# Kernel tuning notes

Hardware: AMD Instinct MI355X
Metric: run time of the kernel (lower is better)

## Reference

```python
import jax, jax.numpy as jnp
import numpy as np

D_MODEL = 2048
N_HEADS = 16
HEAD_DIM = D_MODEL // N_HEADS
B, L = 2, 2048
ROPE_BASE = 10000.0
NEG_INF = -1e30


def _rope_cache(seq_len, head_dim):
    inv_freq = 1.0 / (ROPE_BASE ** (np.arange(0, head_dim, 2, dtype=np.float32) / head_dim))
    t = np.arange(seq_len, dtype=np.float32)
    freqs = np.outer(t, inv_freq)                      # (L, hd/2)
    emb = np.concatenate([freqs, freqs], axis=-1)      # (L, hd)
    return jnp.asarray(np.cos(emb)), jnp.asarray(np.sin(emb))


def setup_inputs() -> dict:
    key = jax.random.key(0)
    kx, kq, ko, kl = jax.random.split(key, 4)
    x = jax.random.normal(kx, (B, L, D_MODEL), dtype=jnp.float32)
    w_qkv = jax.random.normal(kq, (3 * D_MODEL, D_MODEL), dtype=jnp.float32) / np.sqrt(D_MODEL)
    w_out = jax.random.normal(ko, (D_MODEL, D_MODEL), dtype=jnp.float32) / np.sqrt(D_MODEL)
    # key-padding style keep-mask: keep first `lengths[b]` tokens (pos 0 always kept)
    lengths = jax.random.randint(kl, (B,), L // 2, L + 1)
    attn_keep_mask = jnp.arange(L)[None, :] < lengths[:, None]
    cos, sin = _rope_cache(L, HEAD_DIM)
    return {"x": x, "attn_keep_mask": attn_keep_mask, "cos": cos, "sin": sin,
            "w_qkv": w_qkv, "w_out": w_out}


def _rotate_half(t):
    h = t.shape[-1] // 2
    return jnp.concatenate([-t[..., h:], t[..., :h]], axis=-1)


def _apply_rope(t, cos, sin):
    # t: (B, H, L, hd); cos/sin: (L, hd)
    return t * cos[None, None] + _rotate_half(t) * sin[None, None]


def reference(x, attn_keep_mask, cos, sin, w_qkv, w_out):
    Bv, Lv, Dv = x.shape
    qkv = jnp.einsum('bld,ed->ble', x, w_qkv)                      # (B, L, 3D)
    q, k, v = jnp.split(qkv, 3, axis=-1)
    def heads(t):
        return t.reshape(Bv, Lv, N_HEADS, HEAD_DIM).transpose(0, 2, 1, 3)  # (B,H,L,hd)
    q, k, v = heads(q), heads(k), heads(v)
    q = _apply_rope(q, cos, sin)
    k = _apply_rope(k, cos, sin)
    scale = 1.0 / np.sqrt(HEAD_DIM)
    scores = jnp.einsum('bhqd,bhkd->bhqk', q, k) * scale            # (B,H,L,L)
    causal = jnp.tril(jnp.ones((Lv, Lv), dtype=bool))               # (L,L)
    allowed = causal[None, None] & attn_keep_mask[:, None, None, :]  # keep keys
    scores = jnp.where(allowed, scores, NEG_INF)
    probs = jax.nn.softmax(scores, axis=-1)
    attn = jnp.einsum('bhqk,bhkd->bhqd', probs, v)                  # (B,H,L,hd)
    out = attn.transpose(0, 2, 1, 3).reshape(Bv, Lv, Dv)
    out = jnp.where(attn_keep_mask[:, :, None], out, 0.0)
    return jnp.einsum('bld,ed->ble', out, w_out)
```

## Files before the change

kernel.cpp:

```cpp
#include <hip/hip_runtime.h>

typedef unsigned short u16;
typedef u16 u16x8 __attribute__((ext_vector_type(8)));
typedef u16 u16x4 __attribute__((ext_vector_type(4)));
typedef __bf16 bf16x8_t __attribute__((ext_vector_type(8)));
typedef float f32x4 __attribute__((ext_vector_type(4)));

#define GLOBAL_AS __attribute__((address_space(1)))
#define LDS_AS __attribute__((address_space(3)))

__device__ __forceinline__ float bf2f(u16 v) {
    return __uint_as_float(((unsigned int)v) << 16);
}
__device__ __forceinline__ u16 f2bf(float f) {
    unsigned int u = __float_as_uint(f);
    u += 0x7fff + ((u >> 16) & 1);
    return (u16)(u >> 16);
}

__device__ __forceinline__ f32x4 mfma_bf16(u16x8 a, u16x8 b, f32x4 c) {
    return __builtin_amdgcn_mfma_f32_16x16x32_bf16(
        __builtin_bit_cast(bf16x8_t, a), __builtin_bit_cast(bf16x8_t, b), c, 0, 0, 0);
}

__device__ __forceinline__ float red16_max(float x) {
    int t;
    t = __builtin_amdgcn_update_dpp(0, __builtin_bit_cast(int, x), 0xB1, 0xF, 0xF, true);
    x = fmaxf(x, __builtin_bit_cast(float, t));
    t = __builtin_amdgcn_update_dpp(0, __builtin_bit_cast(int, x), 0x4E, 0xF, 0xF, true);
    x = fmaxf(x, __builtin_bit_cast(float, t));
    t = __builtin_amdgcn_update_dpp(0, __builtin_bit_cast(int, x), 0x124, 0xF, 0xF, true);
    x = fmaxf(x, __builtin_bit_cast(float, t));
    t = __builtin_amdgcn_update_dpp(0, __builtin_bit_cast(int, x), 0x128, 0xF, 0xF, true);
    x = fmaxf(x, __builtin_bit_cast(float, t));
    return x;
}

__global__ __launch_bounds__(256) void cvt_kernel(const float* __restrict__ in,
                                                  u16* __restrict__ out, int n4) {
    int i = blockIdx.x * 256 + threadIdx.x;
    if (i >= n4) return;
    float4 f = ((const float4*)in)[i];
    u16x4 o = { f2bf(f.x), f2bf(f.y), f2bf(f.z), f2bf(f.w) };
    ((u16x4*)out)[i] = o;
}

__global__ __launch_bounds__(256) void mask_prep(const unsigned char* __restrict__ raw,
                                                 int* __restrict__ lens) {
    const int b = blockIdx.x;
    const int tid = threadIdx.x, lane = tid & 63, wid = tid >> 6;
    const unsigned char b0 = raw[0];
    int cnt = 0;
    for (int i = tid; i < 2048; i += 256) {
        const size_t idx = (size_t)b * 2048 + i;
        bool v;
        if (b0 == 0) {
            v = ((const float*)raw)[idx] != 0.0f;
        } else if (b0 == 0x80) {
            v = ((const u16*)raw)[idx] != 0;
        } else {
            const int stride = raw[1] ? 1 : (raw[2] ? 2 : (raw[4] ? 4 : 8));
            v = raw[idx * stride] != 0;
        }
        cnt += v ? 1 : 0;
    }
    cnt += __shfl_xor(cnt, 1);
    cnt += __shfl_xor(cnt, 2);
    cnt += __shfl_xor(cnt, 4);
    cnt += __shfl_xor(cnt, 8);
    cnt += __shfl_xor(cnt, 16);
    cnt += __shfl_xor(cnt, 32);
    __shared__ int wsum[4];
    if (lane == 0) wsum[wid] = cnt;
    __syncthreads();
    if (tid == 0) lens[b] = wsum[0] + wsum[1] + wsum[2] + wsum[3];
}

template <int MODE>
__global__ __launch_bounds__(512, 2) void gemm_bt(
    const u16* __restrict__ A, const u16* __restrict__ B,
    int M, int N, int K, int rbx,
    u16* __restrict__ qp, u16* __restrict__ kp, u16* __restrict__ vp,
    float* __restrict__ outf) {
    __shared__ u16 lds[2 * 24576];
    const int tid  = threadIdx.x;
    const int lane = tid & 63;
    const int wid  = tid >> 6;
    const int wr   = wid >> 2;
    const int wc   = wid & 3;

    const int bid = blockIdx.x;
    const int k8  = bid & 7;
    const int loc = bid >> 3;
    const int by  = (k8 >> 2) * 16 + (loc & 15);
    const int bx  = (k8 & 3) * rbx + (loc >> 4);
    const int brow = by * 128;
    const int bcol = bx * 256;

    f32x4 acc[4][4];
#pragma unroll
    for (int m = 0; m < 4; ++m)
#pragma unroll
        for (int n = 0; n < 4; ++n)
            acc[m][n] = (f32x4){0.f, 0.f, 0.f, 0.f};

    const int s5   = (lane & 7) ^ (lane >> 3);
    const int srow = (wid << 4) + 2 * (lane >> 3) + (s5 >> 2);
    const int scol = (s5 & 3) << 3;
    const u16* aS = A + (size_t)(brow + srow) * K + scol;
    const u16* bS = B + (size_t)(bcol + srow) * K + scol;

    auto stgA = [&](int kt, int kh, int bb) {
        __builtin_amdgcn_global_load_lds(
            (const GLOBAL_AS void*)(aS + (size_t)kt * 64 + kh * 32),
            (LDS_AS void*)((char*)lds + bb * 49152 + kh * 8192 + wid * 1024), 16, 0, 0);
    };
    auto stgB = [&](int kt, int kh, int bb) {
        const u16* src = bS + (size_t)kt * 64 + kh * 32;
        char* base = (char*)lds + bb * 49152 + 16384 + kh * 16384 + wid * 1024;
        __builtin_amdgcn_global_load_lds((const GLOBAL_AS void*)src,
            (LDS_AS void*)base, 16, 0, 0);
        __builtin_amdgcn_global_load_lds((const GLOBAL_AS void*)(src + (size_t)128 * K),
            (LDS_AS void*)(base + 8192), 16, 0, 0);
    };

    auto rdA = [&](int bb, int kh, int mi) -> u16x8 {
        const int r  = wr * 64 + mi * 16 + (lane & 15);
        const int pr = r >> 1;
        const int g  = (((r & 1) << 2) + (lane >> 4)) ^ (pr & 7);
        return *(const u16x8*)((const char*)lds + bb * 49152 + kh * 8192 + pr * 128 + g * 16);
    };
    auto rdB = [&](int bb, int kh, int ni) -> u16x8 {
        const int r  = wc * 64 + ni * 16 + (lane & 15);
        const int pr = r >> 1;
        const int g  = (((r & 1) << 2) + (lane >> 4)) ^ (pr & 7);
        return *(const u16x8*)((const char*)lds + bb * 49152 + 16384 + kh * 16384 + pr * 128 + g * 16);
    };

    const int nkt = K >> 6;
    stgA(0, 0, 0); stgB(0, 0, 0);
    stgA(0, 1, 0); stgB(0, 1, 0);

    for (int t = 0; t < nkt; ++t) {
        const int cur = t & 1;
        const bool more = (t + 1 < nkt);
        u16x8 af[4], bf[4];

        asm volatile("s_waitcnt vmcnt(3)" ::: "memory");
        __builtin_amdgcn_s_barrier();
        __builtin_amdgcn_sched_barrier(0);
#pragma unroll
        for (int m = 0; m < 4; ++m) af[m] = rdA(cur, 0, m);
#pragma unroll
        for (int n = 0; n < 4; ++n) bf[n] = rdB(cur, 0, n);
        if (more) { stgA(t + 1, 0, cur ^ 1); stgB(t + 1, 0, cur ^ 1); }
        __builtin_amdgcn_s_setprio(1);
#pragma unroll
        for (int m = 0; m < 4; ++m)
#pragma unroll
            for (int n = 0; n < 4; ++n)
                acc[m][n] = mfma_bf16(af[m], bf[n], acc[m][n]);
        __builtin_amdgcn_s_setprio(0);

        if (more) asm volatile("s_waitcnt vmcnt(3)" ::: "memory");
        else      asm volatile("s_waitcnt vmcnt(0)" ::: "memory");
        __builtin_amdgcn_s_barrier();
        __builtin_amdgcn_sched_barrier(0);
#pragma unroll
        for (int m = 0; m < 4; ++m) af[m] = rdA(cur, 1, m);
#pragma unroll
        for (int n = 0; n < 4; ++n) bf[n] = rdB(cur, 1, n);
        if (more) { stgA(t + 1, 1, cur ^ 1); stgB(t + 1, 1, cur ^ 1); }
        __builtin_amdgcn_s_setprio(1);
#pragma unroll
        for (int m = 0; m < 4; ++m)
#pragma unroll
            for (int n = 0; n < 4; ++n)
                acc[m][n] = mfma_bf16(af[m], bf[n], acc[m][n]);
        __builtin_amdgcn_s_setprio(0);
    }

#pragma unroll
    for (int m = 0; m < 4; ++m) {
#pragma unroll
        for (int n = 0; n < 4; ++n) {
#pragma unroll
            for (int j = 0; j < 4; ++j) {
                const int row = brow + wr * 64 + m * 16 + (lane >> 4) * 4 + j;
                const int col = bcol + wc * 64 + n * 16 + (lane & 15);
                const float val = acc[m][n][j];
                if (MODE == 0) {
                    const int part = col >> 11;
                    const int e = col & 2047;
                    const int hh = e >> 7, dd = e & 127;
                    const int bb = row >> 11, ll = row & 2047;
                    u16* dst = (part == 0) ? qp : (part == 1) ? kp : vp;
                    dst[((size_t)(bb * 16 + hh) * 2048 + ll) * 128 + dd] = f2bf(val);
                } else {
                    outf[(size_t)row * N + col] = val;
                }
            }
        }
    }
}

__global__ __launch_bounds__(256) void rope_kernel(u16* __restrict__ qk,
                                                   const float* __restrict__ cosp,
                                                   const float* __restrict__ sinp) {
    const int gid  = blockIdx.x * 4 + (threadIdx.x >> 6);
    const int lane = threadIdx.x & 63;
    const int l    = gid & 2047;
    u16* row = qk + (size_t)gid * 128;
    const int d1 = lane, d2 = lane + 64;
    const float v1 = bf2f(row[d1]);
    const float v2 = bf2f(row[d2]);
    const float c1 = cosp[l * 128 + d1], s1 = sinp[l * 128 + d1];
    const float c2 = cosp[l * 128 + d2], s2 = sinp[l * 128 + d2];
    row[d1] = f2bf(v1 * c1 - v2 * s1);
    row[d2] = f2bf(v2 * c2 + v1 * s2);
}

__global__ __launch_bounds__(256, 2) void attn_kernel(
    const u16* __restrict__ Q, const u16* __restrict__ K, const u16* __restrict__ V,
    const int* __restrict__ lens, u16* __restrict__ O) {
    __shared__ u16 lK[64 * 128];
    __shared__ u16 lVT[128 * 64];
    __shared__ u16 lP[4 * 16 * 64];

    const int tid = threadIdx.x, lane = tid & 63, wid = tid >> 6;
    const int g   = blockIdx.x;
    const int xcd = g & 7;
    const int r   = g >> 3;
    const int jq  = 31 - (r >> 2);
    const int bh  = (xcd << 2) | (r & 3);
    const int b   = bh >> 4;
    const int h   = bh & 15;
    const u16* qb = Q + (size_t)bh * 2048 * 128;
    const u16* kb = K + (size_t)bh * 2048 * 128;
    const u16* vb = V + (size_t)bh * 2048 * 128;
    const int lenb = lens[b];
    const int q0w = jq * 64 + wid * 16;
    const int str = lane;
    const int sdc = wid;
    const float scale2 = 0.12754245006257017f;
    const float THR = 32.0f;
    u16* lPw = lP + wid * 1024;

    if (jq * 64 >= lenb) {
#pragma unroll
        for (int j = 0; j < 4; ++j) {
            const int qq = q0w + (lane >> 4) * 4 + j;
#pragma unroll
            for (int n = 0; n < 8; ++n) {
                const int d = n * 16 + (lane & 15);
                O[((size_t)b * 2048 + qq) * 2048 + h * 128 + d] = 0;
            }
        }
        return;
    }

    const int nt_full = jq + 1;
    const int lt = (lenb + 63) >> 6;
    const int ktiles = nt_full < lt ? nt_full : lt;

    u16x8 aq[4];
#pragma unroll
    for (int kc = 0; kc < 4; ++kc)
        aq[kc] = *(const u16x8*)(qb + (size_t)(q0w + (lane & 15)) * 128 + kc * 32 + (lane >> 4) * 8);

    u16x8 ONES;
#pragma unroll
    for (int e = 0; e < 8; ++e) ONES[e] = 0x3F80;

    float ms[4];
    f32x4 ls4, alpha4;
    f32x4 ao[8];
#pragma unroll
    for (int j = 0; j < 4; ++j) ms[j] = 0.f;
    ls4 = (f32x4){0.f, 0.f, 0.f, 0.f};
#pragma unroll
    for (int n = 0; n < 8; ++n) ao[n] = (f32x4){0.f, 0.f, 0.f, 0.f};

    u16x8 pk[4], pv[4];
    {
        const u16* ks = kb + (size_t)str * 128 + sdc * 32;
        const u16* vs = vb + (size_t)str * 128 + sdc * 32;
#pragma unroll
        for (int i = 0; i < 4; ++i) { pk[i] = *(const u16x8*)(ks + i * 8); pv[i] = *(const u16x8*)(vs + i * 8); }
    }
#pragma unroll
    for (int i = 0; i < 4; ++i) {
        *(u16x8*)&lK[str * 128 + (((sdc * 4 + i) ^ (str & 7)) << 3)] = pk[i];
#pragma unroll
        for (int e = 0; e < 8; ++e) {
            const int d = sdc * 32 + i * 8 + e;
            lVT[d * 64 + (((str >> 3) ^ (d & 7)) << 3) + (str & 7)] = pv[i][e];
        }
    }
    __syncthreads();

    for (int t = 0; t < ktiles; ++t) {
        const bool pf = (t + 1 < ktiles);
        if (pf) {
            const u16* ks = kb + (size_t)((t + 1) * 64 + str) * 128 + sdc * 32;
            const u16* vs = vb + (size_t)((t + 1) * 64 + str) * 128 + sdc * 32;
#pragma unroll
            for (int i = 0; i < 4; ++i) { pk[i] = *(const u16x8*)(ks + i * 8); pv[i] = *(const u16x8*)(vs + i * 8); }
        }
        const int kv0 = t * 64;

        f32x4 sv4[4];
#pragma unroll
        for (int n = 0; n < 4; ++n) sv4[n] = (f32x4){0.f, 0.f, 0.f, 0.f};
#pragma unroll
        for (int kc = 0; kc < 4; ++kc) {
            u16x8 bk[4];
#pragma unroll
            for (int n = 0; n < 4; ++n) {
                const int rk = n * 16 + (lane & 15);
                bk[n] = *(const u16x8*)&lK[rk * 128 + (((kc * 4 + (lane >> 4)) ^ (rk & 7)) << 3)];
            }
#pragma unroll
            for (int n = 0; n < 4; ++n)
                sv4[n] = mfma_bf16(aq[kc], bk[n], sv4[n]);
        }

        const bool needmask = (t == jq) || (kv0 + 64 > lenb);
#pragma unroll
        for (int j = 0; j < 4; ++j) {
            const int row = (lane >> 4) * 4 + j;
            float sv[4];
            if (needmask) {
                const int qq = q0w + row;
                const int bound = (qq < lenb - 1) ? qq : (lenb - 1);
#pragma unroll
                for (int n = 0; n < 4; ++n) {
                    const int kk = kv0 + n * 16 + (lane & 15);
                    sv[n] = (kk <= bound) ? sv4[n][j] : -1e30f;
                }
            } else {
#pragma unroll
                for (int n = 0; n < 4; ++n) sv[n] = sv4[n][j];
            }
            const float mk = ms[j] * scale2;
#pragma unroll
            for (int n = 0; n < 4; ++n) {
                const float p = exp2f(fmaf(sv[n], scale2, -mk));
                lPw[row * 64 + (((n * 2 + ((lane & 15) >> 3)) ^ (row & 7)) << 3) + (lane & 7)] = f2bf(p);
            }
            const float rm = red16_max(fmaxf(fmaxf(sv[0], sv[1]), fmaxf(sv[2], sv[3])));
            const bool grow = !__all(rm <= ms[j] + THR);
            float a = 1.0f;
            if (grow) {
                const float mn = fmaxf(ms[j], rm);
                a = exp2f((ms[j] - mn) * scale2);
                ms[j] = mn;
            }
            alpha4[j] = a;
        }

#pragma unroll
        for (int kc = 0; kc < 2; ++kc) {
            const int rp = lane & 15;
            u16x8 ap = *(const u16x8*)&lPw[rp * 64 + (((kc * 4 + (lane >> 4)) ^ (rp & 7)) << 3)];
            ls4 = mfma_bf16(ap, ONES, ls4);
#pragma unroll
            for (int n = 0; n < 8; ++n) {
                const int rd = n * 16 + (lane & 15);
                u16x8 bv = *(const u16x8*)&lVT[rd * 64 + (((kc * 4 + (lane >> 4)) ^ (rd & 7)) << 3)];
                ao[n] = mfma_bf16(ap, bv, ao[n]);
            }
        }

        ls4 *= alpha4;
#pragma unroll
        for (int n = 0; n < 8; ++n) ao[n] *= alpha4;

        if (pf) {
            __syncthreads();
#pragma unroll
            for (int i = 0; i < 4; ++i) {
                *(u16x8*)&lK[str * 128 + (((sdc * 4 + i) ^ (str & 7)) << 3)] = pk[i];
#pragma unroll
                for (int e = 0; e < 8; ++e) {
                    const int d = sdc * 32 + i * 8 + e;
                    lVT[d * 64 + (((str >> 3) ^ (d & 7)) << 3) + (str & 7)] = pv[i][e];
                }
            }
            __syncthreads();
        }
    }

#pragma unroll
    for (int j = 0; j < 4; ++j) {
        const int qq = q0w + (lane >> 4) * 4 + j;
        const float inv = (qq < lenb) ? (1.f / ls4[j]) : 0.f;
#pragma unroll
        for (int n = 0; n < 8; ++n) {
            const int d = n * 16 + (lane & 15);
            O[((size_t)b * 2048 + qq) * 2048 + h * 128 + d] = f2bf(ao[n][j] * inv);
        }
    }
}

extern "C" void kernel_launch(void* const* d_in, const int* in_sizes, int n_in,
                              void* d_out, int out_size, void* d_ws, size_t ws_size,
                              hipStream_t stream) {
    const float* x      = (const float*)d_in[0];
    const unsigned char* maskraw = (const unsigned char*)d_in[1];
    const float* cosp   = (const float*)d_in[2];
    const float* sinp   = (const float*)d_in[3];
    const float* w_qkv  = (const float*)d_in[4];
    const float* w_out  = (const float*)d_in[5];
    float* out = (float*)d_out;

    char* ws = (char*)d_ws;
    size_t off = 0;
    auto alloc = [&](size_t bytes) {
        char* p = ws + off;
        off += (bytes + 255) & ~(size_t)255;
        return p;
    };
    u16* xb    = (u16*)alloc((size_t)4096 * 2048 * 2);
    u16* wqkvb = (u16*)alloc((size_t)6144 * 2048 * 2);
    u16* woutb = (u16*)alloc((size_t)2048 * 2048 * 2);
    u16* qB    = (u16*)alloc((size_t)65536 * 128 * 2);
    u16* kB    = (u16*)alloc((size_t)65536 * 128 * 2);
    u16* vB    = (u16*)alloc((size_t)65536 * 128 * 2);
    u16* attno = (u16*)alloc((size_t)4096 * 2048 * 2);
    int* lens  = (int*)alloc(256);

    cvt_kernel<<<dim3(4096 * 2048 / 4 / 256), dim3(256), 0, stream>>>(x, xb, 4096 * 2048 / 4);
    cvt_kernel<<<dim3(6144 * 2048 / 4 / 256), dim3(256), 0, stream>>>(w_qkv, wqkvb, 6144 * 2048 / 4);
    cvt_kernel<<<dim3(2048 * 2048 / 4 / 256), dim3(256), 0, stream>>>(w_out, woutb, 2048 * 2048 / 4);
    mask_prep<<<dim3(2), dim3(256), 0, stream>>>(maskraw, lens);

    gemm_bt<0><<<dim3(768), dim3(512), 0, stream>>>(xb, wqkvb, 4096, 6144, 2048, 6,
                                                    qB, kB, vB, nullptr);
    rope_kernel<<<dim3(131072 / 4), dim3(256), 0, stream>>>(qB, cosp, sinp);
    attn_kernel<<<dim3(1024), dim3(256), 0, stream>>>(qB, kB, vB, lens, attno);
    gemm_bt<1><<<dim3(256), dim3(512), 0, stream>>>(attno, woutb, 4096, 2048, 2048, 2,
                                                    nullptr, nullptr, nullptr, out);
}
```

Baseline: 264.3 us.

## Add dedicated QKV GEMM with 256x384 tiles and triple-buffered LDS pipeline

Replaces the templated QKV projection GEMM (128x256 tiles, 768 blocks, double-buffered) with a dedicated kernel that uses 256x384 tiles over 256 blocks. Loads are staged two k-steps ahead across three LDS buffers, with a swizzled layout. Each wave now computes a 64x192 sub-tile with 48 accumulators, which raises arithmetic intensity per LDS read and cuts global traffic. In exchange, register pressure is much higher and there are fewer blocks to spread over the CUs; 256 blocks roughly matches the CU count, so there may be a tail effect.

```diff
diff --git a/kernel.cpp b/kernel.cpp
--- a/kernel.cpp
+++ b/kernel.cpp
@@ -76,11 +76,124 @@
     if (tid == 0) lens[b] = wsum[0] + wsum[1] + wsum[2] + wsum[3];
 }
 
-template <int MODE>
-__global__ __launch_bounds__(512, 2) void gemm_bt(
+__global__ __launch_bounds__(512, 2) void gemm_qkv(
+    const u16* __restrict__ A, const u16* __restrict__ B, int K,
+    u16* __restrict__ qp, u16* __restrict__ kp, u16* __restrict__ vp) {
+    __shared__ u16 lds[3 * 20480];
+    const int tid  = threadIdx.x;
+    const int lane = tid & 63;
+    const int wid  = tid >> 6;
+    const int wm   = wid & 3;
+    const int wn   = wid >> 2;
+
+    const int bid = blockIdx.x;
+    const int k8  = bid & 7;
+    const int loc = bid >> 3;
+    const int by  = (k8 >> 2) * 8 + (loc & 7);
+    const int bx  = (k8 & 3) * 4 + (loc >> 3);
+    const int brow = by * 256;
+    const int bcol = bx * 384;
+
+    f32x4 acc[4][12];
+#pragma unroll
+    for (int m = 0; m < 4; ++m)
+#pragma unroll
+        for (int n = 0; n < 12; ++n)
+            acc[m][n] = (f32x4){0.f, 0.f, 0.f, 0.f};
+
+    const int s5   = (lane & 7) ^ (lane >> 3);
+    const int rofs = 2 * (lane >> 3) + (s5 >> 2);
+    const int scol = (s5 & 3) << 3;
+
+    const u16* aS0 = A + (size_t)(brow + wid * 32 + rofs) * K + scol;
+    const u16* aS1 = A + (size_t)(brow + wid * 32 + 16 + rofs) * K + scol;
+    const u16* bS0 = B + (size_t)(bcol + wid * 48 + rofs) * K + scol;
+    const u16* bS1 = B + (size_t)(bcol + wid * 48 + 16 + rofs) * K + scol;
+    const u16* bS2 = B + (size_t)(bcol + wid * 48 + 32 + rofs) * K + scol;
+
+    auto stage = [&](int kt, int bb) {
+        char* base = (char*)lds + bb * 40960;
+        const size_t ko = (size_t)kt * 32;
+        __builtin_amdgcn_global_load_lds((const GLOBAL_AS void*)(aS0 + ko),
+            (LDS_AS void*)(base + wid * 2048), 16, 0, 0);
+        __builtin_amdgcn_global_load_lds((const GLOBAL_AS void*)(aS1 + ko),
+            (LDS_AS void*)(base + wid * 2048 + 1024), 16, 0, 0);
+        __builtin_amdgcn_global_load_lds((const GLOBAL_AS void*)(bS0 + ko),
+            (LDS_AS void*)(base + 16384 + wid * 3072), 16, 0, 0);
+        __builtin_amdgcn_global_load_lds((const GLOBAL_AS void*)(bS1 + ko),
+            (LDS_AS void*)(base + 16384 + wid * 3072 + 1024), 16, 0, 0);
+        __builtin_amdgcn_global_load_lds((const GLOBAL_AS void*)(bS2 + ko),
+            (LDS_AS void*)(base + 16384 + wid * 3072 + 2048), 16, 0, 0);
+    };
+
+    auto rdA = [&](int bb, int mi) -> u16x8 {
+        const int r  = wm * 64 + mi * 16 + (lane & 15);
+        const int pr = r >> 1;
+        const int g  = (((r & 1) << 2) + (lane >> 4)) ^ (pr & 7);
+        return *(const u16x8*)((const char*)lds + bb * 40960 + pr * 128 + g * 16);
+    };
+    auto rdB = [&](int bb, int ni) -> u16x8 {
+        const int r  = wn * 192 + ni * 16 + (lane & 15);
+        const int pr = r >> 1;
+        const int g  = (((r & 1) << 2) + (lane >> 4)) ^ (pr & 7);
+        return *(const u16x8*)((const char*)lds + bb * 40960 + 16384 + pr * 128 + g * 16);
+    };
+
+    const int nkt = K >> 5;
+    stage(0, 0);
+    stage(1, 1);
+
+    int bufc = 0;
+    for (int t = 0; t < nkt; ++t) {
+        if (t + 1 < nkt) asm volatile("s_waitcnt vmcnt(5)" ::: "memory");
+        else             asm volatile("s_waitcnt vmcnt(0)" ::: "memory");
+        __builtin_amdgcn_s_barrier();
+        __builtin_amdgcn_sched_barrier(0);
+
+        u16x8 af[4];
+#pragma unroll
+        for (int m = 0; m < 4; ++m) af[m] = rdA(bufc, m);
+
+        if (t + 2 < nkt) {
+            int nb = bufc + 2; if (nb >= 3) nb -= 3;
+            stage(t + 2, nb);
+        }
+
+        __builtin_amdgcn_s_setprio(1);
+#pragma unroll
+        for (int n = 0; n < 12; ++n) {
+            u16x8 bf = rdB(bufc, n);
+#pragma unroll
+            for (int m = 0; m < 4; ++m)
+                acc[m][n] = mfma_bf16(af[m], bf, acc[m][n]);
+        }
+        __builtin_amdgcn_s_setprio(0);
+
+        ++bufc; if (bufc == 3) bufc = 0;
+    }
+
+#pragma unroll
+    for (int m = 0; m < 4; ++m) {
+#pragma unroll
+        for (int n = 0; n < 12; ++n) {
+#pragma unroll
+            for (int j = 0; j < 4; ++j) {
+                const int row = brow + wm * 64 + m * 16 + (lane >> 4) * 4 + j;
+                const int col = bcol + wn * 192 + n * 16 + (lane & 15);
+                const int part = col >> 11;
+                const int e = col & 2047;
+                const int hh = e >> 7, dd = e & 127;
+                const int bb = row >> 11, ll = row & 2047;
+                u16* dst = (part == 0) ? qp : (part == 1) ? kp : vp;
+                dst[((size_t)(bb * 16 + hh) * 2048 + ll) * 128 + dd] = f2bf(acc[m][n][j]);
+            }
+        }
+    }
+}
+
+__global__ __launch_bounds__(512, 2) void gemm_out(
     const u16* __restrict__ A, const u16* __restrict__ B,
     int M, int N, int K, int rbx,
-    u16* __restrict__ qp, u16* __restrict__ kp, u16* __restrict__ vp,
     float* __restrict__ outf) {
     __shared__ u16 lds[2 * 24576];
     const int tid  = threadIdx.x;
@@ -181,27 +294,15 @@
     }
 
 #pragma unroll
-    for (int m = 0; m < 4; ++m) {
-#pragma unroll
-        for (int n = 0; n < 4; ++n) {
+    for (int m = 0; m < 4; ++m)
+#pragma unroll
+        for (int n = 0; n < 4; ++n)
 #pragma unroll
             for (int j = 0; j < 4; ++j) {
                 const int row = brow + wr * 64 + m * 16 + (lane >> 4) * 4 + j;
                 const int col = bcol + wc * 64 + n * 16 + (lane & 15);
-                const float val = acc[m][n][j];
-                if (MODE == 0) {
-                    const int part = col >> 11;
-                    const int e = col & 2047;
-                    const int hh = e >> 7, dd = e & 127;
-                    const int bb = row >> 11, ll = row & 2047;
-                    u16* dst = (part == 0) ? qp : (part == 1) ? kp : vp;
-                    dst[((size_t)(bb * 16 + hh) * 2048 + ll) * 128 + dd] = f2bf(val);
-                } else {
-                    outf[(size_t)row * N + col] = val;
-                }
-            }
-        }
-    }
+                outf[(size_t)row * N + col] = acc[m][n][j];
+            }
 }
 
 __global__ __launch_bounds__(256) void rope_kernel(u16* __restrict__ qk,
@@ -435,10 +536,8 @@
     cvt_kernel<<<dim3(2048 * 2048 / 4 / 256), dim3(256), 0, stream>>>(w_out, woutb, 2048 * 2048 / 4);
     mask_prep<<<dim3(2), dim3(256), 0, stream>>>(maskraw, lens);
 
-    gemm_bt<0><<<dim3(768), dim3(512), 0, stream>>>(xb, wqkvb, 4096, 6144, 2048, 6,
-                                                    qB, kB, vB, nullptr);
+    gemm_qkv<<<dim3(256), dim3(512), 0, stream>>>(xb, wqkvb, 2048, qB, kB, vB);
     rope_kernel<<<dim3(131072 / 4), dim3(256), 0, stream>>>(qB, cosp, sinp);
     attn_kernel<<<dim3(1024), dim3(256), 0, stream>>>(qB, kB, vB, lens, attno);
-    gemm_bt<1><<<dim3(256), dim3(512), 0, stream>>>(attno, woutb, 4096, 2048, 2048, 2,
-                                                    nullptr, nullptr, nullptr, out);
-}
+    gemm_out<<<dim3(256), dim3(512), 0, stream>>>(attno, woutb, 4096, 2048, 2048, 2, out);
+}
```

After: 247.6 us. 1.07x faster.
